# Optimization experiments

Hardware: AMD Instinct MI355X
Metric: run time of the kernel (lower is better)

The kernel has to match this reference:

```python
import jax, jax.numpy as jnp
import numpy as np

NU, NB, NI, D, L = 30000, 10000, 60000, 64, 2
E_UB, E_UI, E_BI = 400000, 800000, 800000


def _graphs(rng, na, nb, ne):
    # random bipartite graph [na, nb] with ne edges; returns Laplacian-normalized
    # symmetric propagation edge list (size 2*ne over na+nb nodes) and the
    # row-normalized aggregation edge values (original MultiCBR preprocessing).
    r = rng.integers(0, na, ne).astype(np.int32)
    c = rng.integers(0, nb, ne).astype(np.int32)
    da = np.bincount(r, minlength=na).astype(np.float32)  # row degrees
    db = np.bincount(c, minlength=nb).astype(np.float32)  # col degrees
    lap = 1.0 / ((np.sqrt(da[r]) + 1e-8) * (np.sqrt(db[c]) + 1e-8))
    prop_rows = np.concatenate([r, c + na]).astype(np.int32)
    prop_cols = np.concatenate([c + na, r]).astype(np.int32)
    prop_vals = np.concatenate([lap, lap]).astype(np.float32)
    agg_vals = (1.0 / (da[r] + 1e-8)).astype(np.float32)  # diag(1/rowsum) @ G
    return prop_rows, prop_cols, prop_vals, r, c, agg_vals


def setup_inputs() -> dict:
    rng = np.random.default_rng(0)
    key = jax.random.key(0)
    ku, kb, ki = jax.random.split(key, 3)
    ub = _graphs(rng, NU, NB, E_UB)
    ui = _graphs(rng, NU, NI, E_UI)
    bi = _graphs(rng, NB, NI, E_BI)
    xav = lambda n: float(np.sqrt(2.0 / (n + D)))  # xavier_normal std
    return {
        "users_feature": jax.random.normal(ku, (NU, D), jnp.float32) * xav(NU),
        "bundles_feature": jax.random.normal(kb, (NB, D), jnp.float32) * xav(NB),
        "items_feature": jax.random.normal(ki, (NI, D), jnp.float32) * xav(NI),
        "ub_rows": jnp.asarray(ub[0]), "ub_cols": jnp.asarray(ub[1]), "ub_vals": jnp.asarray(ub[2]),
        "ui_rows": jnp.asarray(ui[0]), "ui_cols": jnp.asarray(ui[1]), "ui_vals": jnp.asarray(ui[2]),
        "bi_rows": jnp.asarray(bi[0]), "bi_cols": jnp.asarray(bi[1]), "bi_vals": jnp.asarray(bi[2]),
        "bi_agg_rows": jnp.asarray(bi[3]), "bi_agg_cols": jnp.asarray(bi[4]), "bi_agg_vals": jnp.asarray(bi[5]),
        "ui_agg_rows": jnp.asarray(ui[3]), "ui_agg_cols": jnp.asarray(ui[4]), "ui_agg_vals": jnp.asarray(ui[5]),
        "ub_layer_coefs": jnp.full((L + 1,), 1.0 / (L + 1), jnp.float32),
        "ui_layer_coefs": jnp.full((L + 1,), 1.0 / (L + 1), jnp.float32),
        "bi_layer_coefs": jnp.full((L + 1,), 1.0 / (L + 1), jnp.float32),
        "modal_coefs": jnp.asarray([0.4, 0.3, 0.3], jnp.float32),
    }


def _spmm(rows, cols, vals, feat, n):
    # sparse [n, n_src] @ feat : gather + weighted segment-sum
    return jax.ops.segment_sum(vals[:, None] * feat[cols], rows, num_segments=n)


def _l2norm(x):
    # torch F.normalize(p=2, dim=1)
    return x / jnp.maximum(jnp.linalg.norm(x, axis=1, keepdims=True), 1e-12)


def _propagate(rows, cols, vals, a, b, coefs):
    feat = jnp.concatenate([a, b], axis=0)
    n = feat.shape[0]
    acc = coefs[0] * feat  # layer-0 (un-normalized, as in original)
    for i in range(L):
        feat = _spmm(rows, cols, vals, feat, n)
        acc = acc + coefs[i + 1] * _l2norm(feat)
    return acc[: a.shape[0]], acc[a.shape[0]:]


def reference(users_feature, bundles_feature, items_feature,
              ub_rows, ub_cols, ub_vals,
              ui_rows, ui_cols, ui_vals,
              bi_rows, bi_cols, bi_vals,
              bi_agg_rows, bi_agg_cols, bi_agg_vals,
              ui_agg_rows, ui_agg_cols, ui_agg_vals,
              ub_layer_coefs, ui_layer_coefs, bi_layer_coefs, modal_coefs):
    # test=True path of get_multi_modal_representations
    ub_u, ub_b = _propagate(ub_rows, ub_cols, ub_vals, users_feature, bundles_feature, ub_layer_coefs)
    ui_u, ui_i = _propagate(ui_rows, ui_cols, ui_vals, users_feature, items_feature, ui_layer_coefs)
    bi_b, bi_i = _propagate(bi_rows, bi_cols, bi_vals, bundles_feature, items_feature, bi_layer_coefs)
    ui_b = _spmm(bi_agg_rows, bi_agg_cols, bi_agg_vals, ui_i, NB)  # BI_agg @ UI_items
    bi_u = _spmm(ui_agg_rows, ui_agg_cols, ui_agg_vals, bi_i, NU)  # UI_agg @ BI_items
    users_rep = modal_coefs[0] * ub_u + modal_coefs[1] * ui_u + modal_coefs[2] * bi_u
    bundles_rep = modal_coefs[0] * ub_b + modal_coefs[1] * ui_b + modal_coefs[2] * bi_b
    return users_rep, bundles_rep
```

## Files before the change

### kernel.cpp

```cpp
#include <hip/hip_runtime.h>

#define D 64

__device__ __forceinline__ float blo(unsigned u) { return __uint_as_float(u << 16); }
__device__ __forceinline__ float bhi(unsigned u) { return __uint_as_float(u & 0xffff0000u); }
__device__ __forceinline__ unsigned rne(float f) {
    unsigned u = __float_as_uint(f);
    return (u + 0x7fffu + ((u >> 16) & 1u)) >> 16;
}
__device__ __forceinline__ unsigned packbf(float a, float b) {
    unsigned ub = __float_as_uint(b);
    return rne(a) | ((ub + 0x7fffu + ((ub >> 16) & 1u)) & 0xffff0000u);
}
__device__ __forceinline__ void add4(float4* p, float a, float b, float c, float d) {
    float4 o = *p; o.x += a; o.y += b; o.z += c; o.w += d; *p = o;
}

__global__ void to_bf16_kernel(const float* __restrict__ u, const float* __restrict__ b,
                               const float* __restrict__ it,
                               unsigned* __restrict__ SU, unsigned* __restrict__ SB,
                               unsigned* __restrict__ SI, int nU2, int nB2, int nI2) {
    int i = blockIdx.x * 256 + threadIdx.x;
    if (i < nU2) {
        float2 f = ((const float2*)u)[i];
        SU[i] = packbf(f.x, f.y);
    } else if (i < nU2 + nB2) {
        int j = i - nU2;
        float2 f = ((const float2*)b)[j];
        SB[j] = packbf(f.x, f.y);
    } else if (i < nU2 + nB2 + nI2) {
        int j = i - nU2 - nB2;
        float2 f = ((const float2*)it)[j];
        SI[j] = packbf(f.x, f.y);
    }
}

__global__ void hist_kernel(const int* __restrict__ r0, const int* __restrict__ r1,
                            const int* __restrict__ r2,
                            int ne0, int ne1, int ne2, int n0, int n1, int n2,
                            int* __restrict__ histG) {
    __shared__ int h[512];
    int t = threadIdx.x;
    int g = blockIdx.x >> 8, blk = blockIdx.x & 255;
    const int* rows = (g == 0) ? r0 : (g == 1) ? r1 : r2;
    int ne = (g == 0) ? ne0 : (g == 1) ? ne1 : ne2;
    unsigned n = (unsigned)((g == 0) ? n0 : (g == 1) ? n1 : n2);
    h[t] = 0; h[t + 256] = 0;
    __syncthreads();
    int C = (ne + 255) >> 8;
    int e0 = blk * C, e1 = min(ne, e0 + C);
    for (int e = e0 + t; e < e1; e += 256) {
        unsigned b = ((unsigned)rows[e] << 9) / n;
        atomicAdd(&h[b], 1);
    }
    __syncthreads();
    histG[(((g << 9) | t) << 8) | blk] = h[t];
    histG[(((g << 9) | (t + 256)) << 8) | blk] = h[t + 256];
}

__global__ void scan1_kernel(const int* __restrict__ deg, int* __restrict__ rs,
                             int* __restrict__ bsum, int n) {
    __shared__ int tmp[256];
    int t = threadIdx.x;
    int g = blockIdx.x * 256 + t;
    int v = (g < n) ? deg[g] : 0;
    tmp[t] = v;
    __syncthreads();
    for (int off = 1; off < 256; off <<= 1) {
        int x = (t >= off) ? tmp[t - off] : 0;
        __syncthreads();
        tmp[t] += x;
        __syncthreads();
    }
    if (g < n) rs[g] = tmp[t] - v;
    if (t == 255) bsum[blockIdx.x] = tmp[255];
}

__global__ void scan2_kernel(int* __restrict__ bsum, int B) {
    __shared__ int tmp[2048];
    int t = threadIdx.x;
    int v0 = (t < B) ? bsum[t] : 0;
    int v1 = (t + 1024 < B) ? bsum[t + 1024] : 0;
    tmp[t] = v0; tmp[t + 1024] = v1;
    __syncthreads();
    for (int off = 1; off < 2048; off <<= 1) {
        int a0 = (t >= off) ? tmp[t - off] : 0;
        int a1 = ((t + 1024) >= off) ? tmp[t + 1024 - off] : 0;
        __syncthreads();
        tmp[t] += a0; tmp[t + 1024] += a1;
        __syncthreads();
    }
    if (t < B) bsum[t] = tmp[t] - v0;
    if (t + 1024 < B) bsum[t + 1024] = tmp[t + 1024] - v1;
}

__global__ void scan3_kernel(int* __restrict__ rs, const int* __restrict__ bsum, int n) {
    int g = blockIdx.x * blockDim.x + threadIdx.x;
    if (g < n) rs[g] += bsum[g >> 8];
}

__global__ void bucket_scatter_kernel(const int* __restrict__ r0, const int* __restrict__ c0,
                                      const int* __restrict__ r1, const int* __restrict__ c1,
                                      const int* __restrict__ r2, const int* __restrict__ c2,
                                      int ne0, int ne1, int ne2, int n0, int n1, int n2,
                                      const int* __restrict__ hofs, unsigned* __restrict__ ebuf) {
    __shared__ int cur[512];
    int t = threadIdx.x;
    int g = blockIdx.x >> 8, blk = blockIdx.x & 255;
    const int* rows = (g == 0) ? r0 : (g == 1) ? r1 : r2;
    const int* cols = (g == 0) ? c0 : (g == 1) ? c1 : c2;
    int ne = (g == 0) ? ne0 : (g == 1) ? ne1 : ne2;
    int n  = (g == 0) ? n0  : (g == 1) ? n1  : n2;
    cur[t] = hofs[(((g << 9) | t) << 8) | blk];
    cur[t + 256] = hofs[(((g << 9) | (t + 256)) << 8) | blk];
    __syncthreads();
    int C = (ne + 255) >> 8;
    int e0 = blk * C, e1 = min(ne, e0 + C);
    for (int e = e0 + t; e < e1; e += 256) {
        int r = rows[e];
        unsigned b = ((unsigned)r << 9) / (unsigned)n;
        int rb0 = ((int)b * n + 511) >> 9;
        int pos = atomicAdd(&cur[b], 1);
        ebuf[pos] = ((unsigned)(r - rb0) << 23) | (unsigned)cols[e];
    }
}

__global__ void sort_bucket_kernel(const unsigned* __restrict__ ebuf, const int* __restrict__ hofs,
                                   int* __restrict__ rs0, int* __restrict__ rs1, int* __restrict__ rs2,
                                   float* __restrict__ isd0, float* __restrict__ isd1,
                                   float* __restrict__ isd2, int* __restrict__ ccol,
                                   int ne0, int ne1, int ne2, int n0, int n1, int n2) {
    __shared__ int cnt[256];
    __shared__ int pfx[256];
    int t = threadIdx.x;
    int g = blockIdx.x >> 9, b = blockIdx.x & 511;
    int ne = (g == 0) ? ne0 : (g == 1) ? ne1 : ne2;
    int n  = (g == 0) ? n0  : (g == 1) ? n1  : n2;
    int O  = (g == 0) ? 0   : (g == 1) ? ne0 : ne0 + ne1;
    int*   rs  = (g == 0) ? rs0  : (g == 1) ? rs1  : rs2;
    float* isd = (g == 0) ? isd0 : (g == 1) ? isd1 : isd2;
    int rb0 = (b * n + 511) >> 9;
    int rb1 = ((b + 1) * n + 511) >> 9;
    int R = rb1 - rb0;
    cnt[t] = 0;
    __syncthreads();
    int base = hofs[((g << 9) | b) << 8];
    int end  = (b == 511) ? (O + ne) : hofs[((g << 9) | (b + 1)) << 8];
    for (int e = base + t; e < end; e += 256)
        atomicAdd(&cnt[ebuf[e] >> 23], 1);
    __syncthreads();
    pfx[t] = cnt[t];
    __syncthreads();
    for (int off = 1; off < 256; off <<= 1) {
        int v = (t >= off) ? pfx[t - off] : 0;
        __syncthreads();
        pfx[t] += v;
        __syncthreads();
    }
    int c0 = cnt[t], ex = pfx[t] - c0;
    if (t < R) {
        rs[rb0 + t] = base + ex - O;
        isd[rb0 + t] = 1.0f / (sqrtf((float)c0) + 1e-8f);
    }
    __syncthreads();
    cnt[t] = base + ex;
    __syncthreads();
    for (int e = base + t; e < end; e += 256) {
        unsigned p = ebuf[e];
        int pos = atomicAdd(&cnt[p >> 23], 1);
        ccol[pos] = (int)(p & 0x7fffffu);
    }
    if (b == 511 && t == 0) rs[n] = ne;
}

struct GA {
    const int* rs; const int* ccol; const float* isd;
    const unsigned* srcA; const unsigned* srcB; int na;
    const float* inA; const float* inB;
    unsigned* feat_out; float* dst0; void* dst1;
    const float* coefs; const float* modalp; int mi; int n;
};

template <bool FIRST, bool A0, bool A1, bool BF16D1>
__global__ void spmm_norm_kernel(GA A, GA B, int ntot) {
    int lane = threadIdx.x & 63;
    int row = (blockIdx.x * (blockDim.x >> 6) + (threadIdx.x >> 6)) * 8 + (lane >> 3);
    if (row >= ntot) return;
    GA G; int r;
    if (row < A.n) { G = A; r = row; }
    else           { G = B; r = row - A.n; if (r >= G.n) return; }
    int q = lane & 7;
    int s = G.rs[r], e = G.rs[r + 1];
    float isr = G.isd[r];
    const unsigned* src; int coff;
    if (FIRST && r < G.na) { src = G.srcB; coff = G.na; }
    else                   { src = G.srcA; coff = 0; }
    src += (q << 2);
    const int* cc = G.ccol;
    const float* isdp = G.isd;
    float a[8];
#pragma unroll
    for (int j = 0; j < 8; ++j) a[j] = 0.f;
    int k = s;
    for (; k + 1 < e; k += 2) {
        int c0 = cc[k], c1 = cc[k + 1];
        uint4 f0 = *(const uint4*)(src + (size_t)(c0 - coff) * 32);
        uint4 f1 = *(const uint4*)(src + (size_t)(c1 - coff) * 32);
        if (FIRST) {
            float v0 = isdp[c0], v1 = isdp[c1];
            a[0] = fmaf(v0, blo(f0.x), a[0]); a[1] = fmaf(v0, bhi(f0.x), a[1]);
            a[2] = fmaf(v0, blo(f0.y), a[2]); a[3] = fmaf(v0, bhi(f0.y), a[3]);
            a[4] = fmaf(v0, blo(f0.z), a[4]); a[5] = fmaf(v0, bhi(f0.z), a[5]);
            a[6] = fmaf(v0, blo(f0.w), a[6]); a[7] = fmaf(v0, bhi(f0.w), a[7]);
            a[0] = fmaf(v1, blo(f1.x), a[0]); a[1] = fmaf(v1, bhi(f1.x), a[1]);
            a[2] = fmaf(v1, blo(f1.y), a[2]); a[3] = fmaf(v1, bhi(f1.y), a[3]);
            a[4] = fmaf(v1, blo(f1.z), a[4]); a[5] = fmaf(v1, bhi(f1.z), a[5]);
            a[6] = fmaf(v1, blo(f1.w), a[6]); a[7] = fmaf(v1, bhi(f1.w), a[7]);
        } else {
            a[0] += blo(f0.x) + blo(f1.x); a[1] += bhi(f0.x) + bhi(f1.x);
            a[2] += blo(f0.y) + blo(f1.y); a[3] += bhi(f0.y) + bhi(f1.y);
            a[4] += blo(f0.z) + blo(f1.z); a[5] += bhi(f0.z) + bhi(f1.z);
            a[6] += blo(f0.w) + blo(f1.w); a[7] += bhi(f0.w) + bhi(f1.w);
        }
    }
    if (k < e) {
        int c0 = cc[k];
        uint4 f0 = *(const uint4*)(src + (size_t)(c0 - coff) * 32);
        if (FIRST) {
            float v0 = isdp[c0];
            a[0] = fmaf(v0, blo(f0.x), a[0]); a[1] = fmaf(v0, bhi(f0.x), a[1]);
            a[2] = fmaf(v0, blo(f0.y), a[2]); a[3] = fmaf(v0, bhi(f0.y), a[3]);
            a[4] = fmaf(v0, blo(f0.z), a[4]); a[5] = fmaf(v0, bhi(f0.z), a[5]);
            a[6] = fmaf(v0, blo(f0.w), a[6]); a[7] = fmaf(v0, bhi(f0.w), a[7]);
        } else {
            a[0] += blo(f0.x); a[1] += bhi(f0.x);
            a[2] += blo(f0.y); a[3] += bhi(f0.y);
            a[4] += blo(f0.z); a[5] += bhi(f0.z);
            a[6] += blo(f0.w); a[7] += bhi(f0.w);
        }
    }
    float s2 = 0.f;
#pragma unroll
    for (int j = 0; j < 8; ++j) s2 += a[j] * a[j];
    s2 += __shfl_xor(s2, 1, 64);
    s2 += __shfl_xor(s2, 2, 64);
    s2 += __shfl_xor(s2, 4, 64);
    float inv = 1.0f / fmaxf(sqrtf(s2), 1e-12f);
    float mm = G.modalp[G.mi];
    size_t ro = (size_t)r * D + (q << 3);
    float ctb[8];
    if (FIRST) {
        float isr2 = isr * isr;
        uint4 fw;
        fw.x = packbf(isr2 * a[0], isr2 * a[1]);
        fw.y = packbf(isr2 * a[2], isr2 * a[3]);
        fw.z = packbf(isr2 * a[4], isr2 * a[5]);
        fw.w = packbf(isr2 * a[6], isr2 * a[7]);
        *(uint4*)(G.feat_out + (size_t)r * 32 + (q << 2)) = fw;
        const float* ib = (r < G.na) ? (G.inA + ro) : (G.inB + (size_t)(r - G.na) * D + (q << 3));
        float4 a0 = *(const float4*)ib;
        float4 a1 = *(const float4*)(ib + 4);
        float c0 = G.coefs[0], c1m = G.coefs[1] * inv;
        ctb[0] = mm * fmaf(c0, a0.x, c1m * a[0]);
        ctb[1] = mm * fmaf(c0, a0.y, c1m * a[1]);
        ctb[2] = mm * fmaf(c0, a0.z, c1m * a[2]);
        ctb[3] = mm * fmaf(c0, a0.w, c1m * a[3]);
        ctb[4] = mm * fmaf(c0, a1.x, c1m * a[4]);
        ctb[5] = mm * fmaf(c0, a1.y, c1m * a[5]);
        ctb[6] = mm * fmaf(c0, a1.z, c1m * a[6]);
        ctb[7] = mm * fmaf(c0, a1.w, c1m * a[7]);
    } else {
        float mc = mm * G.coefs[2] * inv;
#pragma unroll
        for (int j = 0; j < 8; ++j) ctb[j] = mc * a[j];
    }
    if (r < G.na) {
        if (A0) {
            *(float4*)(G.dst0 + ro) = make_float4(ctb[0], ctb[1], ctb[2], ctb[3]);
            *(float4*)(G.dst0 + ro + 4) = make_float4(ctb[4], ctb[5], ctb[6], ctb[7]);
        } else {
            add4((float4*)(G.dst0 + ro), ctb[0], ctb[1], ctb[2], ctb[3]);
            add4((float4*)(G.dst0 + ro + 4), ctb[4], ctb[5], ctb[6], ctb[7]);
        }
    } else if (BF16D1) {
        unsigned* p = (unsigned*)G.dst1 + (size_t)(r - G.na) * 32 + (q << 2);
        if (!A1) {
            uint4 cur = *(const uint4*)p;
            ctb[0] += blo(cur.x); ctb[1] += bhi(cur.x);
            ctb[2] += blo(cur.y); ctb[3] += bhi(cur.y);
            ctb[4] += blo(cur.z); ctb[5] += bhi(cur.z);
            ctb[6] += blo(cur.w); ctb[7] += bhi(cur.w);
        }
        uint4 w;
        w.x = packbf(ctb[0], ctb[1]); w.y = packbf(ctb[2], ctb[3]);
        w.z = packbf(ctb[4], ctb[5]); w.w = packbf(ctb[6], ctb[7]);
        *(uint4*)p = w;
    } else {
        float* d1 = (float*)G.dst1 + (size_t)(r - G.na) * D + (q << 3);
        add4((float4*)d1, ctb[0], ctb[1], ctb[2], ctb[3]);
        add4((float4*)(d1 + 4), ctb[4], ctb[5], ctb[6], ctb[7]);
    }
}

__global__ void agg2_kernel(const int* __restrict__ rsA, const int* __restrict__ ccA,
                            const unsigned* __restrict__ sA, float* __restrict__ oA,
                            int naA, int nA,
                            const int* __restrict__ rsB, const int* __restrict__ ccB,
                            const unsigned* __restrict__ sB, float* __restrict__ oB,
                            int naB, int nB) {
    int lane = threadIdx.x & 63;
    int row = (blockIdx.x * (blockDim.x >> 6) + (threadIdx.x >> 6)) * 8 + (lane >> 3);
    if (row >= nA + nB) return;
    const int* rs; const int* cc; const unsigned* src; float* out; int na; int r;
    if (row < nA) { rs = rsA; cc = ccA; src = sA; out = oA; na = naA; r = row; }
    else          { rs = rsB; cc = ccB; src = sB; out = oB; na = naB; r = row - nA; }
    int q = lane & 7;
    src += (q << 2);
    int s = rs[r], e = rs[r + 1];
    float a[8];
#pragma unroll
    for (int j = 0; j < 8; ++j) a[j] = 0.f;
    int k = s;
    for (; k + 1 < e; k += 2) {
        int c0 = cc[k] - na, c1 = cc[k + 1] - na;
        uint4 f0 = *(const uint4*)(src + (size_t)c0 * 32);
        uint4 f1 = *(const uint4*)(src + (size_t)c1 * 32);
        a[0] += blo(f0.x) + blo(f1.x); a[1] += bhi(f0.x) + bhi(f1.x);
        a[2] += blo(f0.y) + blo(f1.y); a[3] += bhi(f0.y) + bhi(f1.y);
        a[4] += blo(f0.z) + blo(f1.z); a[5] += bhi(f0.z) + bhi(f1.z);
        a[6] += blo(f0.w) + blo(f1.w); a[7] += bhi(f0.w) + bhi(f1.w);
    }
    if (k < e) {
        int c0 = cc[k] - na;
        uint4 f0 = *(const uint4*)(src + (size_t)c0 * 32);
        a[0] += blo(f0.x); a[1] += bhi(f0.x);
        a[2] += blo(f0.y); a[3] += bhi(f0.y);
        a[4] += blo(f0.z); a[5] += bhi(f0.z);
        a[6] += blo(f0.w); a[7] += bhi(f0.w);
    }
    float ad = 1.0f / ((float)(e - s) + 1e-8f);
    float* p = out + (size_t)r * D + (q << 3);
    add4((float4*)p, ad * a[0], ad * a[1], ad * a[2], ad * a[3]);
    add4((float4*)(p + 4), ad * a[4], ad * a[5], ad * a[6], ad * a[7]);
}

extern "C" void kernel_launch(void* const* d_in, const int* in_sizes, int n_in,
                              void* d_out, int out_size, void* d_ws, size_t ws_size,
                              hipStream_t stream) {
    const float* users   = (const float*)d_in[0];
    const float* bundles = (const float*)d_in[1];
    const float* items   = (const float*)d_in[2];
    const int*   ub_rows = (const int*)d_in[3];
    const int*   ub_cols = (const int*)d_in[4];
    const int*   ui_rows = (const int*)d_in[6];
    const int*   ui_cols = (const int*)d_in[7];
    const int*   bi_rows = (const int*)d_in[9];
    const int*   bi_cols = (const int*)d_in[10];
    const float* ub_coefs = (const float*)d_in[18];
    const float* ui_coefs = (const float*)d_in[19];
    const float* bi_coefs = (const float*)d_in[20];
    const float* modal    = (const float*)d_in[21];

    const int NU_ = in_sizes[0] / D;
    const int NB_ = in_sizes[1] / D;
    const int NI_ = in_sizes[2] / D;
    const int ne_ub = in_sizes[3];
    const int ne_ui = in_sizes[6];
    const int ne_bi = in_sizes[9];

    const int n_ui = NU_ + NI_;
    const int n_bi = NB_ + NI_;
    const int n_ub = NU_ + NB_;

    float* out = (float*)d_out;

    int*      rs_ui  = (int*)d_ws;
    int*      rs_bi  = rs_ui + 90112;
    int*      rs_ub  = rs_bi + 70144;
    float*    isd_ui = (float*)(rs_ub + 40192);
    float*    isd_bi = isd_ui + 90112;
    float*    isd_ub = isd_bi + 70144;
    int*      hofs   = (int*)(isd_ub + 40192);
    int*      bsum   = hofs + 393280;
    int*      ccol   = bsum + 2048;
    int*      histG  = ccol;
    unsigned* SU     = (unsigned*)(ccol + 4000000);
    unsigned* SB     = SU + 960000;
    unsigned* SI     = SB + 320000;
    unsigned* ovl    = SI + 1920000;
    unsigned* ebuf   = ovl;
    unsigned* sfB_ui = ovl;
    unsigned* sfB_bi = sfB_ui + 2880000;
    unsigned* IT1b   = sfB_bi + 2240000;
    unsigned* IT2b   = IT1b + 1920000;
    unsigned* sfB_ub = IT1b;

    int* ccol_ui = ccol;
    int* ccol_bi = ccol + ne_ui;
    int* ccol_ub = ccol + ne_ui + ne_bi;

    float* out_u = out;
    float* out_b = out + (size_t)NU_ * D;

    {
        int tot2 = (NU_ + NB_ + NI_) * 32;
        to_bf16_kernel<<<(tot2 + 255) / 256, 256, 0, stream>>>(
            users, bundles, items, SU, SB, SI, NU_ * 32, NB_ * 32, NI_ * 32);
    }

    hist_kernel<<<768, 256, 0, stream>>>(ui_rows, bi_rows, ub_rows,
                                         ne_ui, ne_bi, ne_ub, n_ui, n_bi, n_ub, histG);
    scan1_kernel<<<1536, 256, 0, stream>>>(histG, hofs, bsum, 393216);
    scan2_kernel<<<1, 1024, 0, stream>>>(bsum, 1536);
    scan3_kernel<<<1536, 256, 0, stream>>>(hofs, bsum, 393216);
    bucket_scatter_kernel<<<768, 256, 0, stream>>>(
        ui_rows, ui_cols, bi_rows, bi_cols, ub_rows, ub_cols,
        ne_ui, ne_bi, ne_ub, n_ui, n_bi, n_ub, hofs, ebuf);
    sort_bucket_kernel<<<1536, 256, 0, stream>>>(
        ebuf, hofs, rs_ui, rs_bi, rs_ub, isd_ui, isd_bi, isd_ub, ccol,
        ne_ui, ne_bi, ne_ub, n_ui, n_bi, n_ub);

    GA gUI = { rs_ui, ccol_ui, isd_ui, SU, SI, NU_, users, items,
               sfB_ui, out_u, (void*)IT1b, ui_coefs, modal, 1, n_ui };
    GA gBI = { rs_bi, ccol_bi, isd_bi, SB, SI, NB_, bundles, items,
               sfB_bi, out_b, (void*)IT2b, bi_coefs, modal, 2, n_bi };
    GA gUB = { rs_ub, ccol_ub, isd_ub, SU, SB, NU_, users, bundles,
               sfB_ub, out_u, (void*)out_b, ub_coefs, modal, 0, n_ub };
    GA gUI2 = gUI; gUI2.srcA = sfB_ui;
    GA gBI2 = gBI; gBI2.srcA = sfB_bi;
    GA gUB2 = gUB; gUB2.srcA = sfB_ub;

    int ntotL = n_ui + n_bi;
    spmm_norm_kernel<true,  true,  true,  true ><<<(ntotL + 31) / 32, 256, 0, stream>>>(gUI,  gBI,  ntotL);
    spmm_norm_kernel<false, false, false, true ><<<(ntotL + 31) / 32, 256, 0, stream>>>(gUI2, gBI2, ntotL);

    agg2_kernel<<<(NU_ + NB_ + 31) / 32, 256, 0, stream>>>(
        rs_ui, ccol_ui, IT2b, out_u, NU_, NU_,
        rs_bi, ccol_bi, IT1b, out_b, NB_, NB_);

    spmm_norm_kernel<true,  false, false, false><<<(n_ub + 31) / 32, 256, 0, stream>>>(gUB,  gUB,  n_ub);
    spmm_norm_kernel<false, false, false, false><<<(n_ub + 31) / 32, 256, 0, stream>>>(gUB2, gUB2, n_ub);
}
```

Baseline: 493.7 us.

## Sort rows by degree before SpMM to balance wavefront work

Adds a per-graph degree histogram, scan and scatter that build a permutation ordering rows by descending degree (capped at 255). All SpMM and aggregation kernels then process rows through this permutation, so the eight rows sharing a wavefront have similar lengths and less lane divergence. The cost is four extra small kernel launches, an indirection load per row, and less locality in output writes.

Result: slower. 533.5 us (+8.1%).

```diff
diff --git a/kernel.cpp b/kernel.cpp
--- a/kernel.cpp
+++ b/kernel.cpp
@@ -173,6 +173,83 @@
     if (b == 511 && t == 0) rs[n] = ne;
 }
 
+__device__ __forceinline__ int row_deg(int list, int r, const int* rs_ui, const int* rs_bi,
+                                       const int* rs_ub, int n_ui, int NU) {
+    const int* rs; int rr;
+    if (list == 0) { if (r < n_ui) { rs = rs_ui; rr = r; } else { rs = rs_bi; rr = r - n_ui; } }
+    else if (list == 1) { rs = rs_ub; rr = r; }
+    else { if (r < NU) { rs = rs_ui; rr = r; } else { rs = rs_bi; rr = r - NU; } }
+    return rs[rr + 1] - rs[rr];
+}
+
+__global__ void zero768_kernel(int* __restrict__ p) { p[threadIdx.x] = 0; }
+
+__global__ void deg_hist_kernel(const int* __restrict__ rs_ui, const int* __restrict__ rs_bi,
+                                const int* __restrict__ rs_ub,
+                                int n_ui, int NU, int n0, int n1, int n2,
+                                int b0, int b1, int* __restrict__ hist) {
+    __shared__ int h[256];
+    int t = threadIdx.x;
+    h[t] = 0;
+    __syncthreads();
+    int blk = blockIdx.x, list, base, n;
+    if (blk < b0)           { list = 0; base = blk;           n = n0; }
+    else if (blk < b0 + b1) { list = 1; base = blk - b0;      n = n1; }
+    else                    { list = 2; base = blk - b0 - b1; n = n2; }
+    int r = base * 256 + t;
+    if (r < n) {
+        int d = row_deg(list, r, rs_ui, rs_bi, rs_ub, n_ui, NU);
+        int bin = 255 - min(d, 255);
+        atomicAdd(&h[bin], 1);
+    }
+    __syncthreads();
+    if (h[t]) atomicAdd(&hist[list * 256 + t], h[t]);
+}
+
+__global__ void deg_scan_kernel(const int* __restrict__ hist, int* __restrict__ gcur) {
+    __shared__ int tmp[256];
+    int t = threadIdx.x;
+    for (int l = 0; l < 3; ++l) {
+        int v = hist[l * 256 + t];
+        tmp[t] = v;
+        __syncthreads();
+        for (int off = 1; off < 256; off <<= 1) {
+            int x = (t >= off) ? tmp[t - off] : 0;
+            __syncthreads();
+            tmp[t] += x;
+            __syncthreads();
+        }
+        gcur[l * 256 + t] = tmp[t] - v;
+        __syncthreads();
+    }
+}
+
+__global__ void deg_scatter_kernel(const int* __restrict__ rs_ui, const int* __restrict__ rs_bi,
+                                   const int* __restrict__ rs_ub,
+                                   int n_ui, int NU, int n0, int n1, int n2,
+                                   int b0, int b1, int* __restrict__ gcur, int* __restrict__ perm) {
+    __shared__ int lcnt[256];
+    __shared__ int lbase[256];
+    int t = threadIdx.x;
+    lcnt[t] = 0;
+    __syncthreads();
+    int blk = blockIdx.x, list, base, n, pbase;
+    if (blk < b0)           { list = 0; base = blk;           n = n0; pbase = 0; }
+    else if (blk < b0 + b1) { list = 1; base = blk - b0;      n = n1; pbase = n0; }
+    else                    { list = 2; base = blk - b0 - b1; n = n2; pbase = n0 + n1; }
+    int r = base * 256 + t, bin = 0, my = 0;
+    bool ok = (r < n);
+    if (ok) {
+        int d = row_deg(list, r, rs_ui, rs_bi, rs_ub, n_ui, NU);
+        bin = 255 - min(d, 255);
+        my = atomicAdd(&lcnt[bin], 1);
+    }
+    __syncthreads();
+    if (lcnt[t]) lbase[t] = atomicAdd(&gcur[list * 256 + t], lcnt[t]);
+    __syncthreads();
+    if (ok) perm[pbase + lbase[bin] + my] = r;
+}
+
 struct GA {
     const int* rs; const int* ccol; const float* isd;
     const unsigned* srcA; const unsigned* srcB; int na;
@@ -182,10 +259,11 @@
 };
 
 template <bool FIRST, bool A0, bool A1, bool BF16D1>
-__global__ void spmm_norm_kernel(GA A, GA B, int ntot) {
+__global__ void spmm_norm_kernel(GA A, GA B, const int* __restrict__ perm, int ntot) {
     int lane = threadIdx.x & 63;
     int row = (blockIdx.x * (blockDim.x >> 6) + (threadIdx.x >> 6)) * 8 + (lane >> 3);
     if (row >= ntot) return;
+    row = perm[row];
     GA G; int r;
     if (row < A.n) { G = A; r = row; }
     else           { G = B; r = row - A.n; if (r >= G.n) return; }
@@ -307,10 +385,11 @@
                             int naA, int nA,
                             const int* __restrict__ rsB, const int* __restrict__ ccB,
                             const unsigned* __restrict__ sB, float* __restrict__ oB,
-                            int naB, int nB) {
+                            int naB, int nB, const int* __restrict__ perm) {
     int lane = threadIdx.x & 63;
     int row = (blockIdx.x * (blockDim.x >> 6) + (threadIdx.x >> 6)) * 8 + (lane >> 3);
     if (row >= nA + nB) return;
+    row = perm[row];
     const int* rs; const int* cc; const unsigned* src; float* out; int na; int r;
     if (row < nA) { rs = rsA; cc = ccA; src = sA; out = oA; na = naA; r = row; }
     else          { rs = rsB; cc = ccB; src = sB; out = oB; na = naB; r = row - nA; }
@@ -399,6 +478,13 @@
     int* ccol_bi = ccol + ne_ui;
     int* ccol_ub = ccol + ne_ui + ne_bi;
 
+    const int n0 = n_ui + n_bi, n1 = n_ub, n2 = NU_ + NB_;
+    int* perm0 = hofs;
+    int* perm1 = perm0 + n0;
+    int* perm2 = perm1 + n1;
+    int* dhist = (int*)ovl;
+    int* dgcur = dhist + 768;
+
     float* out_u = out;
     float* out_b = out + (size_t)NU_ * D;
 
@@ -420,6 +506,16 @@
         ebuf, hofs, rs_ui, rs_bi, rs_ub, isd_ui, isd_bi, isd_ub, ccol,
         ne_ui, ne_bi, ne_ub, n_ui, n_bi, n_ub);
 
+    {
+        int b0 = (n0 + 255) >> 8, b1 = (n1 + 255) >> 8, b2 = (n2 + 255) >> 8;
+        zero768_kernel<<<1, 768, 0, stream>>>(dhist);
+        deg_hist_kernel<<<b0 + b1 + b2, 256, 0, stream>>>(
+            rs_ui, rs_bi, rs_ub, n_ui, NU_, n0, n1, n2, b0, b1, dhist);
+        deg_scan_kernel<<<1, 256, 0, stream>>>(dhist, dgcur);
+        deg_scatter_kernel<<<b0 + b1 + b2, 256, 0, stream>>>(
+            rs_ui, rs_bi, rs_ub, n_ui, NU_, n0, n1, n2, b0, b1, dgcur, perm0);
+    }
+
     GA gUI = { rs_ui, ccol_ui, isd_ui, SU, SI, NU_, users, items,
                sfB_ui, out_u, (void*)IT1b, ui_coefs, modal, 1, n_ui };
     GA gBI = { rs_bi, ccol_bi, isd_bi, SB, SI, NB_, bundles, items,
@@ -431,13 +527,13 @@
     GA gUB2 = gUB; gUB2.srcA = sfB_ub;
 
     int ntotL = n_ui + n_bi;
-    spmm_norm_kernel<true,  true,  true,  true ><<<(ntotL + 31) / 32, 256, 0, stream>>>(gUI,  gBI,  ntotL);
-    spmm_norm_kernel<false, false, false, true ><<<(ntotL + 31) / 32, 256, 0, stream>>>(gUI2, gBI2, ntotL);
+    spmm_norm_kernel<true,  true,  true,  true ><<<(ntotL + 31) / 32, 256, 0, stream>>>(gUI,  gBI,  perm0, ntotL);
+    spmm_norm_kernel<false, false, false, true ><<<(ntotL + 31) / 32, 256, 0, stream>>>(gUI2, gBI2, perm0, ntotL);
 
     agg2_kernel<<<(NU_ + NB_ + 31) / 32, 256, 0, stream>>>(
         rs_ui, ccol_ui, IT2b, out_u, NU_, NU_,
-        rs_bi, ccol_bi, IT1b, out_b, NB_, NB_);
-
-    spmm_norm_kernel<true,  false, false, false><<<(n_ub + 31) / 32, 256, 0, stream>>>(gUB,  gUB,  n_ub);
-    spmm_norm_kernel<false, false, false, false><<<(n_ub + 31) / 32, 256, 0, stream>>>(gUB2, gUB2, n_ub);
-}
+        rs_bi, ccol_bi, IT1b, out_b, NB_, NB_, perm2);
+
+    spmm_norm_kernel<true,  false, false, false><<<(n_ub + 31) / 32, 256, 0, stream>>>(gUB,  gUB,  perm1, n_ub);
+    spmm_norm_kernel<false, false, false, false><<<(n_ub + 31) / 32, 256, 0, stream>>>(gUB2, gUB2, perm1, n_ub);
+}
```

## Degree-sort rows within windows for load balance; unroll gather loops by four

Applied to the files above, without the earlier changes.

Adds a windowed counting-sort kernel that orders rows by descending degree inside 2048-row windows, so the eight rows handled by each wavefront have similar degrees. The SpMM and aggregation kernels read rows through this permutation. Their gather loops are unrolled by four to keep more loads in flight, and launch bounds are set. The cost is an extra kernel and an indirection per row. The permutation also breaks the contiguity of output writes, and the perm buffers reuse the hofs scratch space.

After: 520.2 us. +5.4%, slower.

```diff
diff --git a/kernel.cpp b/kernel.cpp
--- a/kernel.cpp
+++ b/kernel.cpp
@@ -1,6 +1,7 @@
 #include <hip/hip_runtime.h>
 
 #define D 64
+#define WIN 2048
 
 __device__ __forceinline__ float blo(unsigned u) { return __uint_as_float(u << 16); }
 __device__ __forceinline__ float bhi(unsigned u) { return __uint_as_float(u & 0xffff0000u); }
@@ -173,6 +174,59 @@
     if (b == 511 && t == 0) rs[n] = ne;
 }
 
+__device__ __forceinline__ int row_deg(int list, int r, const int* rs_ui, const int* rs_bi,
+                                       const int* rs_ub, int n_ui, int NU) {
+    const int* rs; int rr;
+    if (list == 0) { if (r < n_ui) { rs = rs_ui; rr = r; } else { rs = rs_bi; rr = r - n_ui; } }
+    else if (list == 1) { rs = rs_ub; rr = r; }
+    else { if (r < NU) { rs = rs_ui; rr = r; } else { rs = rs_bi; rr = r - NU; } }
+    return rs[rr + 1] - rs[rr];
+}
+
+__global__ void winsort_kernel(const int* __restrict__ rs_ui, const int* __restrict__ rs_bi,
+                               const int* __restrict__ rs_ub,
+                               int n_ui, int NU, int n0, int n1, int n2,
+                               int w0, int w1,
+                               int* __restrict__ perm0, int* __restrict__ perm1,
+                               int* __restrict__ perm2) {
+    __shared__ int hist[256];
+    __shared__ int pfx[256];
+    int t = threadIdx.x;
+    int blk = blockIdx.x, list, wbase, n; int* perm;
+    if (blk < w0)           { list = 0; wbase = blk * WIN;             n = n0; perm = perm0; }
+    else if (blk < w0 + w1) { list = 1; wbase = (blk - w0) * WIN;      n = n1; perm = perm1; }
+    else                    { list = 2; wbase = (blk - w0 - w1) * WIN; n = n2; perm = perm2; }
+    hist[t] = 0;
+    __syncthreads();
+    int lim = min(n - wbase, WIN);
+    int bins[8], ranks[8];
+#pragma unroll
+    for (int i = 0; i < 8; ++i) {
+        int rr = i * 256 + t;
+        if (rr < lim) {
+            int d = row_deg(list, wbase + rr, rs_ui, rs_bi, rs_ub, n_ui, NU);
+            int b = 255 - min(d, 255);
+            bins[i] = b;
+            ranks[i] = atomicAdd(&hist[b], 1);
+        } else bins[i] = -1;
+    }
+    __syncthreads();
+    int h = hist[t];
+    pfx[t] = h;
+    __syncthreads();
+    for (int off = 1; off < 256; off <<= 1) {
+        int x = (t >= off) ? pfx[t - off] : 0;
+        __syncthreads();
+        pfx[t] += x;
+        __syncthreads();
+    }
+    hist[t] = pfx[t] - h;
+    __syncthreads();
+#pragma unroll
+    for (int i = 0; i < 8; ++i)
+        if (bins[i] >= 0) perm[wbase + hist[bins[i]] + ranks[i]] = wbase + i * 256 + t;
+}
+
 struct GA {
     const int* rs; const int* ccol; const float* isd;
     const unsigned* srcA; const unsigned* srcB; int na;
@@ -182,10 +236,12 @@
 };
 
 template <bool FIRST, bool A0, bool A1, bool BF16D1>
-__global__ void spmm_norm_kernel(GA A, GA B, int ntot) {
+__launch_bounds__(256, 8)
+__global__ void spmm_norm_kernel(GA A, GA B, const int* __restrict__ perm, int ntot) {
     int lane = threadIdx.x & 63;
     int row = (blockIdx.x * (blockDim.x >> 6) + (threadIdx.x >> 6)) * 8 + (lane >> 3);
     if (row >= ntot) return;
+    row = perm[row];
     GA G; int r;
     if (row < A.n) { G = A; r = row; }
     else           { G = B; r = row - A.n; if (r >= G.n) return; }
@@ -202,6 +258,41 @@
 #pragma unroll
     for (int j = 0; j < 8; ++j) a[j] = 0.f;
     int k = s;
+    for (; k + 3 < e; k += 4) {
+        int c0 = cc[k], c1 = cc[k + 1], c2 = cc[k + 2], c3 = cc[k + 3];
+        uint4 f0 = *(const uint4*)(src + (size_t)(c0 - coff) * 32);
+        uint4 f1 = *(const uint4*)(src + (size_t)(c1 - coff) * 32);
+        uint4 f2 = *(const uint4*)(src + (size_t)(c2 - coff) * 32);
+        uint4 f3 = *(const uint4*)(src + (size_t)(c3 - coff) * 32);
+        if (FIRST) {
+            float v0 = isdp[c0], v1 = isdp[c1], v2 = isdp[c2], v3 = isdp[c3];
+            a[0] = fmaf(v0, blo(f0.x), a[0]); a[1] = fmaf(v0, bhi(f0.x), a[1]);
+            a[2] = fmaf(v0, blo(f0.y), a[2]); a[3] = fmaf(v0, bhi(f0.y), a[3]);
+            a[4] = fmaf(v0, blo(f0.z), a[4]); a[5] = fmaf(v0, bhi(f0.z), a[5]);
+            a[6] = fmaf(v0, blo(f0.w), a[6]); a[7] = fmaf(v0, bhi(f0.w), a[7]);
+            a[0] = fmaf(v1, blo(f1.x), a[0]); a[1] = fmaf(v1, bhi(f1.x), a[1]);
+            a[2] = fmaf(v1, blo(f1.y), a[2]); a[3] = fmaf(v1, bhi(f1.y), a[3]);
+            a[4] = fmaf(v1, blo(f1.z), a[4]); a[5] = fmaf(v1, bhi(f1.z), a[5]);
+            a[6] = fmaf(v1, blo(f1.w), a[6]); a[7] = fmaf(v1, bhi(f1.w), a[7]);
+            a[0] = fmaf(v2, blo(f2.x), a[0]); a[1] = fmaf(v2, bhi(f2.x), a[1]);
+            a[2] = fmaf(v2, blo(f2.y), a[2]); a[3] = fmaf(v2, bhi(f2.y), a[3]);
+            a[4] = fmaf(v2, blo(f2.z), a[4]); a[5] = fmaf(v2, bhi(f2.z), a[5]);
+            a[6] = fmaf(v2, blo(f2.w), a[6]); a[7] = fmaf(v2, bhi(f2.w), a[7]);
+            a[0] = fmaf(v3, blo(f3.x), a[0]); a[1] = fmaf(v3, bhi(f3.x), a[1]);
+            a[2] = fmaf(v3, blo(f3.y), a[2]); a[3] = fmaf(v3, bhi(f3.y), a[3]);
+            a[4] = fmaf(v3, blo(f3.z), a[4]); a[5] = fmaf(v3, bhi(f3.z), a[5]);
+            a[6] = fmaf(v3, blo(f3.w), a[6]); a[7] = fmaf(v3, bhi(f3.w), a[7]);
+        } else {
+            a[0] += blo(f0.x) + blo(f1.x); a[1] += bhi(f0.x) + bhi(f1.x);
+            a[2] += blo(f0.y) + blo(f1.y); a[3] += bhi(f0.y) + bhi(f1.y);
+            a[4] += blo(f0.z) + blo(f1.z); a[5] += bhi(f0.z) + bhi(f1.z);
+            a[6] += blo(f0.w) + blo(f1.w); a[7] += bhi(f0.w) + bhi(f1.w);
+            a[0] += blo(f2.x) + blo(f3.x); a[1] += bhi(f2.x) + bhi(f3.x);
+            a[2] += blo(f2.y) + blo(f3.y); a[3] += bhi(f2.y) + bhi(f3.y);
+            a[4] += blo(f2.z) + blo(f3.z); a[5] += bhi(f2.z) + bhi(f3.z);
+            a[6] += blo(f2.w) + blo(f3.w); a[7] += bhi(f2.w) + bhi(f3.w);
+        }
+    }
     for (; k + 1 < e; k += 2) {
         int c0 = cc[k], c1 = cc[k + 1];
         uint4 f0 = *(const uint4*)(src + (size_t)(c0 - coff) * 32);
@@ -302,15 +393,17 @@
     }
 }
 
+__launch_bounds__(256, 8)
 __global__ void agg2_kernel(const int* __restrict__ rsA, const int* __restrict__ ccA,
                             const unsigned* __restrict__ sA, float* __restrict__ oA,
                             int naA, int nA,
                             const int* __restrict__ rsB, const int* __restrict__ ccB,
                             const unsigned* __restrict__ sB, float* __restrict__ oB,
-                            int naB, int nB) {
+                            int naB, int nB, const int* __restrict__ perm) {
     int lane = threadIdx.x & 63;
     int row = (blockIdx.x * (blockDim.x >> 6) + (threadIdx.x >> 6)) * 8 + (lane >> 3);
     if (row >= nA + nB) return;
+    row = perm[row];
     const int* rs; const int* cc; const unsigned* src; float* out; int na; int r;
     if (row < nA) { rs = rsA; cc = ccA; src = sA; out = oA; na = naA; r = row; }
     else          { rs = rsB; cc = ccB; src = sB; out = oB; na = naB; r = row - nA; }
@@ -321,6 +414,21 @@
 #pragma unroll
     for (int j = 0; j < 8; ++j) a[j] = 0.f;
     int k = s;
+    for (; k + 3 < e; k += 4) {
+        int c0 = cc[k] - na, c1 = cc[k + 1] - na, c2 = cc[k + 2] - na, c3 = cc[k + 3] - na;
+        uint4 f0 = *(const uint4*)(src + (size_t)c0 * 32);
+        uint4 f1 = *(const uint4*)(src + (size_t)c1 * 32);
+        uint4 f2 = *(const uint4*)(src + (size_t)c2 * 32);
+        uint4 f3 = *(const uint4*)(src + (size_t)c3 * 32);
+        a[0] += blo(f0.x) + blo(f1.x); a[1] += bhi(f0.x) + bhi(f1.x);
+        a[2] += blo(f0.y) + blo(f1.y); a[3] += bhi(f0.y) + bhi(f1.y);
+        a[4] += blo(f0.z) + blo(f1.z); a[5] += bhi(f0.z) + bhi(f1.z);
+        a[6] += blo(f0.w) + blo(f1.w); a[7] += bhi(f0.w) + bhi(f1.w);
+        a[0] += blo(f2.x) + blo(f3.x); a[1] += bhi(f2.x) + bhi(f3.x);
+        a[2] += blo(f2.y) + blo(f3.y); a[3] += bhi(f2.y) + bhi(f3.y);
+        a[4] += blo(f2.z) + blo(f3.z); a[5] += bhi(f2.z) + bhi(f3.z);
+        a[6] += blo(f2.w) + blo(f3.w); a[7] += bhi(f2.w) + bhi(f3.w);
+    }
     for (; k + 1 < e; k += 2) {
         int c0 = cc[k] - na, c1 = cc[k + 1] - na;
         uint4 f0 = *(const uint4*)(src + (size_t)c0 * 32);
@@ -399,6 +507,11 @@
     int* ccol_bi = ccol + ne_ui;
     int* ccol_ub = ccol + ne_ui + ne_bi;
 
+    const int n0 = n_ui + n_bi, n1 = n_ub, n2 = NU_ + NB_;
+    int* perm0 = hofs;
+    int* perm1 = perm0 + n0;
+    int* perm2 = perm1 + n1;
+
     float* out_u = out;
     float* out_b = out + (size_t)NU_ * D;
 
@@ -420,6 +533,12 @@
         ebuf, hofs, rs_ui, rs_bi, rs_ub, isd_ui, isd_bi, isd_ub, ccol,
         ne_ui, ne_bi, ne_ub, n_ui, n_bi, n_ub);
 
+    {
+        int w0 = (n0 + WIN - 1) / WIN, w1 = (n1 + WIN - 1) / WIN, w2 = (n2 + WIN - 1) / WIN;
+        winsort_kernel<<<w0 + w1 + w2, 256, 0, stream>>>(
+            rs_ui, rs_bi, rs_ub, n_ui, NU_, n0, n1, n2, w0, w1, perm0, perm1, perm2);
+    }
+
     GA gUI = { rs_ui, ccol_ui, isd_ui, SU, SI, NU_, users, items,
                sfB_ui, out_u, (void*)IT1b, ui_coefs, modal, 1, n_ui };
     GA gBI = { rs_bi, ccol_bi, isd_bi, SB, SI, NB_, bundles, items,
@@ -431,13 +550,13 @@
     GA gUB2 = gUB; gUB2.srcA = sfB_ub;
 
     int ntotL = n_ui + n_bi;
-    spmm_norm_kernel<true,  true,  true,  true ><<<(ntotL + 31) / 32, 256, 0, stream>>>(gUI,  gBI,  ntotL);
-    spmm_norm_kernel<false, false, false, true ><<<(ntotL + 31) / 32, 256, 0, stream>>>(gUI2, gBI2, ntotL);
+    spmm_norm_kernel<true,  true,  true,  true ><<<(ntotL + 31) / 32, 256, 0, stream>>>(gUI,  gBI,  perm0, ntotL);
+    spmm_norm_kernel<false, false, false, true ><<<(ntotL + 31) / 32, 256, 0, stream>>>(gUI2, gBI2, perm0, ntotL);
 
     agg2_kernel<<<(NU_ + NB_ + 31) / 32, 256, 0, stream>>>(
         rs_ui, ccol_ui, IT2b, out_u, NU_, NU_,
-        rs_bi, ccol_bi, IT1b, out_b, NB_, NB_);
-
-    spmm_norm_kernel<true,  false, false, false><<<(n_ub + 31) / 32, 256, 0, stream>>>(gUB,  gUB,  n_ub);
-    spmm_norm_kernel<false, false, false, false><<<(n_ub + 31) / 32, 256, 0, stream>>>(gUB2, gUB2, n_ub);
-}
+        rs_bi, ccol_bi, IT1b, out_b, NB_, NB_, perm2);
+
+    spmm_norm_kernel<true,  false, false, false><<<(n_ub + 31) / 32, 256, 0, stream>>>(gUB,  gUB,  perm1, n_ub);
+    spmm_norm_kernel<false, false, false, false><<<(n_ub + 31) / 32, 256, 0, stream>>>(gUB2, gUB2, perm1, n_ub);
+}
```
